# Performance work log

Hardware: AMD Instinct MI355X
Metric: run time of the kernel (lower is better)

The kernel has to match this reference:

```python
import jax, jax.numpy as jnp
import numpy as np

N_NODES = 100000
N_EDGES = 1600000
N_LABEL = 200000
IN_CH, HID_CH, OUT_CH = 64, 128, 64


def setup_inputs() -> dict:
    key = jax.random.key(0)
    ks = jax.random.split(key, 9)
    glorot = lambda k, fi, fo: jax.random.normal(k, (fi, fo), jnp.float32) * (2.0 / (fi + fo)) ** 0.5
    return {
        "x": jax.random.normal(ks[0], (N_NODES, IN_CH), jnp.float32),
        "W_l1": glorot(ks[1], IN_CH, HID_CH),
        "W_r1": glorot(ks[2], IN_CH, HID_CH),
        "b1": jnp.zeros((HID_CH,), jnp.float32),
        "W_l2": glorot(ks[3], HID_CH, OUT_CH),
        "W_r2": glorot(ks[4], HID_CH, OUT_CH),
        "b2": jnp.zeros((OUT_CH,), jnp.float32),
        "edge_index": jax.random.randint(ks[5], (2, N_EDGES), 0, N_NODES, jnp.int64 if jax.config.jax_enable_x64 else jnp.int32),
        "edge_label_index": jax.random.randint(ks[6], (2, N_LABEL), 0, N_NODES, jnp.int64 if jax.config.jax_enable_x64 else jnp.int32),
    }


def _sage_conv(x, edge_index, W_l, W_r, b):
    # PyG SAGEConv (mean aggr): out = lin_l(mean_{j in N(i)} x_j) + lin_r(x_i)
    src, dst = edge_index[0], edge_index[1]
    msg = x[src]                                             # [E, d] gather
    agg = jax.ops.segment_sum(msg, dst, num_segments=x.shape[0])  # [N, d]
    cnt = jax.ops.segment_sum(jnp.ones((edge_index.shape[1], 1), x.dtype), dst,
                              num_segments=x.shape[0])       # [N, 1]
    mean = agg / jnp.maximum(cnt, 1.0)                       # isolated nodes -> 0
    return mean @ W_l + x @ W_r + b


def reference(x, W_l1, W_r1, b1, W_l2, W_r2, b2, edge_index, edge_label_index):
    # encode (inference mode: dropout is identity)
    h = jax.nn.relu(_sage_conv(x, edge_index, W_l1, W_r1, b1))
    z = _sage_conv(h, edge_index, W_l2, W_r2, b2)            # [N, out]
    # decode: dot-product link scores
    src = z[edge_label_index[0]]                             # [P, out]
    dst = z[edge_label_index[1]]
    return jnp.sum(src * dst, axis=-1)                       # [P]
```

## Files before the change

### kernel.cpp

```cpp
#include <hip/hip_runtime.h>
#include <hip/hip_bf16.h>


#define NBUCK 512
#define NPB   200
#define WI    64

typedef __attribute__((ext_vector_type(2))) float f32x2;
typedef __attribute__((ext_vector_type(4))) float f32x4;
typedef __attribute__((ext_vector_type(4))) int i32x4;
typedef __attribute__((ext_vector_type(2))) unsigned int u32x2;
typedef __attribute__((ext_vector_type(4))) unsigned short u16x4;
typedef __attribute__((ext_vector_type(8))) unsigned short u16x8;
typedef __attribute__((ext_vector_type(8))) short s16x8;

__device__ inline unsigned short f2bf(float f) {
    unsigned u = __float_as_uint(f);
    u += 0x7fffu + ((u >> 16) & 1u);
    return (unsigned short)(u >> 16);
}
__device__ inline float bf2f(unsigned short h) {
    return __uint_as_float(((unsigned)h) << 16);
}
__device__ inline unsigned int pk4_fp8(float a, float b, float c, float d) {
    int w = __builtin_amdgcn_cvt_pk_fp8_f32(a, b, 0, false);
    w = __builtin_amdgcn_cvt_pk_fp8_f32(c, d, w, true);
    return (unsigned int)w;
}
__device__ inline unsigned char one_fp8(float a) {
    return (unsigned char)(__builtin_amdgcn_cvt_pk_fp8_f32(a, a, 0, false) & 0xFF);
}
__device__ inline void acc_fp8(unsigned int a, f32x2& lo, f32x2& hi) {
#if __has_builtin(__builtin_amdgcn_cvt_pk_f32_fp8)
    lo += __builtin_amdgcn_cvt_pk_f32_fp8((int)a, false);
    hi += __builtin_amdgcn_cvt_pk_f32_fp8((int)a, true);
#else
    lo.x += __builtin_amdgcn_cvt_f32_fp8((int)a, 0);
    lo.y += __builtin_amdgcn_cvt_f32_fp8((int)a, 1);
    hi.x += __builtin_amdgcn_cvt_f32_fp8((int)a, 2);
    hi.y += __builtin_amdgcn_cvt_f32_fp8((int)a, 3);
#endif
}

__global__ __launch_bounds__(256) void k_prep(const float* __restrict__ x,
                                              const float* __restrict__ Wl1,
                                              const float* __restrict__ Wr1,
                                              const float* __restrict__ Wl2,
                                              const float* __restrict__ Wr2,
                                              unsigned short* __restrict__ w1t,
                                              unsigned short* __restrict__ w2t,
                                              unsigned short* __restrict__ xb,
                                              unsigned int* __restrict__ xq,
                                              int* __restrict__ meta,
                                              long long nx) {
    if (blockIdx.x < 16) {
        if (blockIdx.x == 0) {
            i32x4 z = {0, 0, 0, 0};
            *(i32x4*)(meta + threadIdx.x * 4) = z;
        }
        int id = (blockIdx.x * 256 + threadIdx.x) * 8;
        int which = id >> 14;
        int r0 = id & 16383;
#pragma unroll
        for (int i = 0; i < 8; ++i) {
            int r = r0 + i;
            int n = r >> 7, k = r & 127;
            float v;
            if (which == 0) v = (k < 64) ? Wl1[k * 128 + n] : Wr1[(k - 64) * 128 + n];
            else            v = (n < 64) ? Wl2[k * 64 + n] : Wr2[k * 64 + (n - 64)];
            (which ? w2t : w1t)[r] = f2bf(v);
        }
        return;
    }
    long long i = ((long long)(blockIdx.x - 16) * 256 + threadIdx.x) * 8;
    if (i + 8 > nx) return;
    f32x4 a = __builtin_nontemporal_load((const f32x4*)(x + i));
    f32x4 b = __builtin_nontemporal_load((const f32x4*)(x + i + 4));
    u16x8 o;
    o[0] = f2bf(a.x); o[1] = f2bf(a.y); o[2] = f2bf(a.z); o[3] = f2bf(a.w);
    o[4] = f2bf(b.x); o[5] = f2bf(b.y); o[6] = f2bf(b.z); o[7] = f2bf(b.w);
    __builtin_nontemporal_store(o, (u16x8*)(xb + i));
    u32x2 q;
    q.x = pk4_fp8(a.x, a.y, a.z, a.w);
    q.y = pk4_fp8(b.x, b.y, b.z, b.w);
    __builtin_nontemporal_store(q, (u32x2*)(xq + (i >> 2)));
}

__global__ __launch_bounds__(256) void k_bucket(const int* __restrict__ ei, int E,
                                                int capB,
                                                int* __restrict__ buckets,
                                                int* __restrict__ meta,
                                                int* __restrict__ ovfA) {
    __shared__ int lcnt[NBUCK];
    __shared__ int lbase[NBUCK];
    __shared__ int lidx[NBUCK];
    const int t = threadIdx.x;
    const int e0 = blockIdx.x * 4096;
    for (int i = t; i < NBUCK; i += 256) { lcnt[i] = 0; lidx[i] = 0; }
    __syncthreads();

    int s[16], d[16], b[16];
    bool v[16];
#pragma unroll
    for (int r = 0; r < 4; ++r) {
        int e = e0 + r * 1024 + t * 4;
        i32x4 s4, d4;
        if (e + 4 <= E) {
            s4 = __builtin_nontemporal_load((const i32x4*)(ei + e));
            d4 = __builtin_nontemporal_load((const i32x4*)(ei + E + e));
        } else {
            s4.x = (e < E) ? ei[e] : 0;         d4.x = (e < E) ? ei[E + e] : 0;
            s4.y = (e + 1 < E) ? ei[e + 1] : 0; d4.y = (e + 1 < E) ? ei[E + e + 1] : 0;
            s4.z = (e + 2 < E) ? ei[e + 2] : 0; d4.z = (e + 2 < E) ? ei[E + e + 2] : 0;
            s4.w = (e + 3 < E) ? ei[e + 3] : 0; d4.w = (e + 3 < E) ? ei[E + e + 3] : 0;
        }
        s[r * 4 + 0] = s4.x; s[r * 4 + 1] = s4.y; s[r * 4 + 2] = s4.z; s[r * 4 + 3] = s4.w;
        d[r * 4 + 0] = d4.x; d[r * 4 + 1] = d4.y; d[r * 4 + 2] = d4.z; d[r * 4 + 3] = d4.w;
        v[r * 4 + 0] = (e < E); v[r * 4 + 1] = (e + 1 < E);
        v[r * 4 + 2] = (e + 2 < E); v[r * 4 + 3] = (e + 3 < E);
    }
#pragma unroll
    for (int k = 0; k < 16; ++k) {
        b[k] = (unsigned)d[k] / NPB;
        if (v[k]) atomicAdd(&lcnt[b[k]], 1);
    }
    __syncthreads();
    for (int i = t; i < NBUCK; i += 256) {
        int c = lcnt[i];
        lbase[i] = (c > 0) ? atomicAdd(&meta[i], c) : 0;
    }
    __syncthreads();
#pragma unroll
    for (int k = 0; k < 16; ++k) {
        if (!v[k]) continue;
        int slot = atomicAdd(&lidx[b[k]], 1);
        int pos = lbase[b[k]] + slot;
        if (pos < capB) {
            int local = d[k] - b[k] * NPB;
            buckets[(size_t)b[k] * capB + pos] = (local << 17) | s[k];
        } else {
            int oi = atomicAdd(&meta[NBUCK], 1);
            ovfA[(size_t)oi * 2] = s[k];
            ovfA[(size_t)oi * 2 + 1] = d[k];
        }
    }
}

__global__ __launch_bounds__(256) void k_fill_lds(const int* __restrict__ buckets,
                                                  int capB,
                                                  const int* __restrict__ meta_ro,
                                                  int* __restrict__ deg,
                                                  int* __restrict__ ell, int N) {
    __shared__ int cur[NPB];
    __shared__ int ells[NPB * WI];
    const int t = threadIdx.x;
    const int b = blockIdx.x;
    const int base = b * NPB;
    for (int i = t; i < NPB; i += 256) cur[i] = 0;
    __syncthreads();
    const int cnt = min(meta_ro[b], capB);
    const int* bk = buckets + (size_t)b * capB;
    for (int i = t; i < cnt; i += 256) {
        unsigned v = (unsigned)__builtin_nontemporal_load(bk + i);
        int s = (int)(v & 0x1FFFFu);
        int local = (int)(v >> 17);
        int slot = atomicAdd(&cur[local], 1);
        if (slot < WI) ells[local * WI + slot] = s;
    }
    __syncthreads();
    const int nn = min(NPB, N - base);
    if (nn <= 0) return;
    for (int i = t; i < nn; i += 256) deg[base + i] = cur[i];
    const int lim = nn * WI;
    for (int j = t * 4; j < lim; j += 256 * 4) {
        if ((j & (WI - 1)) >= cur[j >> 6]) continue;
        i32x4 vv = *(const i32x4*)&ells[j];
        __builtin_nontemporal_store(vv, (i32x4*)(ell + (size_t)base * WI + j));
    }
}

__global__ __launch_bounds__(256) void k_fill_list(const int* __restrict__ ovfA,
                                                   const int* __restrict__ meta_ro,
                                                   int* __restrict__ deg,
                                                   int* __restrict__ ell) {
    const int cnt = meta_ro[NBUCK];
    for (int i = blockIdx.x * 256 + threadIdx.x; i < cnt; i += gridDim.x * 256) {
        int s = ovfA[(size_t)i * 2];
        int d = ovfA[(size_t)i * 2 + 1];
        int pos = atomicAdd(&deg[d], 1);
        if (pos < WI) ell[(size_t)d * WI + pos] = s;
    }
}

__global__ __launch_bounds__(256) void k_agg_q(const unsigned int* __restrict__ featq,
                                               const int* __restrict__ deg,
                                               const int* __restrict__ ell,
                                               unsigned short* __restrict__ outb,
                                               const float* __restrict__ addend,
                                               int n) {
    const int node = blockIdx.x * 16 + (threadIdx.x >> 4);
    const int l = threadIdx.x & 15;
    if (node >= n) return;
    const int dg = deg[node];
    const int cnt = min(dg, WI);
    const int* row = ell + (size_t)node * WI;
    f32x2 lo = {0.f, 0.f}, hi = {0.f, 0.f};
    int j = 0;
    for (; j + 8 <= cnt; j += 8) {
        i32x4 sA = __builtin_nontemporal_load((const i32x4*)(row + j));
        i32x4 sB = __builtin_nontemporal_load((const i32x4*)(row + j + 4));
        unsigned a0 = featq[(size_t)sA.x * 16 + l];
        unsigned a1 = featq[(size_t)sA.y * 16 + l];
        unsigned a2 = featq[(size_t)sA.z * 16 + l];
        unsigned a3 = featq[(size_t)sA.w * 16 + l];
        unsigned a4 = featq[(size_t)sB.x * 16 + l];
        unsigned a5 = featq[(size_t)sB.y * 16 + l];
        unsigned a6 = featq[(size_t)sB.z * 16 + l];
        unsigned a7 = featq[(size_t)sB.w * 16 + l];
        acc_fp8(a0, lo, hi); acc_fp8(a1, lo, hi);
        acc_fp8(a2, lo, hi); acc_fp8(a3, lo, hi);
        acc_fp8(a4, lo, hi); acc_fp8(a5, lo, hi);
        acc_fp8(a6, lo, hi); acc_fp8(a7, lo, hi);
    }
    if (j + 4 <= cnt) {
        i32x4 sA = __builtin_nontemporal_load((const i32x4*)(row + j));
        unsigned a0 = featq[(size_t)sA.x * 16 + l];
        unsigned a1 = featq[(size_t)sA.y * 16 + l];
        unsigned a2 = featq[(size_t)sA.z * 16 + l];
        unsigned a3 = featq[(size_t)sA.w * 16 + l];
        acc_fp8(a0, lo, hi); acc_fp8(a1, lo, hi);
        acc_fp8(a2, lo, hi); acc_fp8(a3, lo, hi);
        j += 4;
    }
    for (; j < cnt; ++j) {
        int s = __builtin_nontemporal_load(row + j);
        acc_fp8(featq[(size_t)s * 16 + l], lo, hi);
    }
    const float inv = 1.0f / (float)max(dg, 1);
    float vx = lo.x * inv, vy = lo.y * inv, vz = hi.x * inv, vw = hi.y * inv;
    if (addend) {
        const f32x4 ad = *(const f32x4*)(addend + (size_t)node * 64 + l * 4);
        vx += ad.x; vy += ad.y; vz += ad.z; vw += ad.w;
    }
    u16x4 ob;
    ob[0] = f2bf(vx); ob[1] = f2bf(vy); ob[2] = f2bf(vz); ob[3] = f2bf(vw);
    __builtin_nontemporal_store(ob, (u16x4*)(outb + (size_t)node * 64 + l * 4));
}

__global__ __launch_bounds__(256) void k_gemm_fused(
    const unsigned short* __restrict__ mean1b,
    const unsigned short* __restrict__ xb,
    const unsigned short* __restrict__ w1t,
    const unsigned short* __restrict__ w2t,
    const float* __restrict__ b1,
    const float* __restrict__ b2,
    unsigned int* __restrict__ pq,
    float* __restrict__ zb, int M) {
    __shared__ unsigned short W1s[128 * 128];
    __shared__ unsigned short W2s[128 * 128];
    __shared__ __align__(16) unsigned short HT[128 * 136];
    const int t = threadIdx.x;
    const int wv = t >> 6, l = t & 63;
    const int lr = l & 15, lq = l >> 4;
    const int wrow = wv * 32;
    const int row0 = blockIdx.x * 128 + wrow;

    const s16x8 zf = {0, 0, 0, 0, 0, 0, 0, 0};
    s16x8 af[2][4];
#pragma unroll
    for (int mt = 0; mt < 2; ++mt) {
        int r = row0 + mt * 16 + lr;
        bool ok = r < M;
#pragma unroll
        for (int ks = 0; ks < 4; ++ks) {
            int k = ks * 32 + lq * 8;
            const unsigned short* src = (k < 64) ? (mean1b + (size_t)r * 64 + k)
                                                 : (xb + (size_t)r * 64 + (k - 64));
            af[mt][ks] = ok ? *(const s16x8*)src : zf;
        }
    }
#pragma unroll
    for (int i = 0; i < 8; ++i) {
        int byte = (i * 256 + t) * 16;
        int swz = byte ^ (((byte >> 8) & 7) << 4);
        *(u16x8*)((char*)W1s + swz) = *(const u16x8*)((const char*)w1t + byte);
        *(u16x8*)((char*)W2s + swz) = *(const u16x8*)((const char*)w2t + byte);
    }
    __syncthreads();
    if (row0 >= M) return;

    f32x4 acc[2][8];
#pragma unroll
    for (int mt = 0; mt < 2; ++mt)
#pragma unroll
        for (int nt = 0; nt < 8; ++nt) {
            f32x4 z = {0.f, 0.f, 0.f, 0.f};
            acc[mt][nt] = z;
        }
#pragma unroll
    for (int nt = 0; nt < 8; ++nt) {
        int n = nt * 16 + lr;
#pragma unroll
        for (int ks = 0; ks < 4; ++ks) {
            int byte = (n * 256 + ks * 64 + lq * 16) ^ ((n & 7) << 4);
            s16x8 bf = *(const s16x8*)((const char*)W1s + byte);
            acc[0][nt] = __builtin_amdgcn_mfma_f32_16x16x32_bf16(af[0][ks], bf, acc[0][nt], 0, 0, 0);
            acc[1][nt] = __builtin_amdgcn_mfma_f32_16x16x32_bf16(af[1][ks], bf, acc[1][nt], 0, 0, 0);
        }
    }
#pragma unroll
    for (int nt = 0; nt < 8; ++nt) {
        float bb = b1[nt * 16 + lr];
#pragma unroll
        for (int mt = 0; mt < 2; ++mt)
#pragma unroll
            for (int j = 0; j < 4; ++j) {
                float v = fmaxf(acc[mt][nt][j] + bb, 0.f);
                HT[(wrow + mt * 16 + lq * 4 + j) * 136 + nt * 16 + lr] = f2bf(v);
            }
    }
    s16x8 af2[2][4];
#pragma unroll
    for (int mt = 0; mt < 2; ++mt)
#pragma unroll
        for (int ks = 0; ks < 4; ++ks)
            af2[mt][ks] = *(const s16x8*)&HT[(wrow + mt * 16 + lr) * 136 + ks * 32 + lq * 8];

    f32x4 acc2[2][8];
#pragma unroll
    for (int mt = 0; mt < 2; ++mt)
#pragma unroll
        for (int nt = 0; nt < 8; ++nt) {
            f32x4 z = {0.f, 0.f, 0.f, 0.f};
            acc2[mt][nt] = z;
        }
#pragma unroll
    for (int nt = 0; nt < 8; ++nt) {
        int n = nt * 16 + lr;
#pragma unroll
        for (int ks = 0; ks < 4; ++ks) {
            int byte = (n * 256 + ks * 64 + lq * 16) ^ ((n & 7) << 4);
            s16x8 bf = *(const s16x8*)((const char*)W2s + byte);
            acc2[0][nt] = __builtin_amdgcn_mfma_f32_16x16x32_bf16(af2[0][ks], bf, acc2[0][nt], 0, 0, 0);
            acc2[1][nt] = __builtin_amdgcn_mfma_f32_16x16x32_bf16(af2[1][ks], bf, acc2[1][nt], 0, 0, 0);
        }
    }
    char* scratch = (char*)&HT[(size_t)wrow * 136];
    unsigned char* csb = (unsigned char*)scratch;
#pragma unroll
    for (int nt = 0; nt < 4; ++nt)
#pragma unroll
        for (int mt = 0; mt < 2; ++mt)
#pragma unroll
            for (int j = 0; j < 4; ++j)
                csb[(mt * 16 + lq * 4 + j) * 68 + nt * 16 + lr] = one_fp8(acc2[mt][nt][j]);
#pragma unroll
    for (int p = 0; p < 8; ++p) {
        int r = p * 4 + lq;
        int gr = row0 + r;
        if (gr < M) {
            unsigned int v = *(const unsigned int*)&csb[r * 68 + lr * 4];
            __builtin_nontemporal_store(v, pq + (size_t)gr * 16 + lr);
        }
    }
    __syncthreads();
    float* csf = (float*)scratch;
#pragma unroll
    for (int nt = 4; nt < 8; ++nt) {
        int col = (nt - 4) * 16 + lr;
        float bb = b2[col];
#pragma unroll
        for (int mt = 0; mt < 2; ++mt)
#pragma unroll
            for (int j = 0; j < 4; ++j)
                csf[(mt * 16 + lq * 4 + j) * 68 + col] = acc2[mt][nt][j] + bb;
    }
#pragma unroll
    for (int p = 0; p < 8; ++p) {
        int r = p * 4 + lq;
        int gr = row0 + r;
        if (gr < M) {
            f32x4 v = *(const f32x4*)&csf[r * 68 + lr * 4];
            __builtin_nontemporal_store(v, (f32x4*)(zb + (size_t)gr * 64 + lr * 4));
        }
    }
}

__global__ __launch_bounds__(256) void k_decode(const unsigned short* __restrict__ zq,
                                                const int* __restrict__ eli,
                                                float* __restrict__ out, int P) {
    int t = threadIdx.x;
    int g = blockIdx.x * 16 + (t >> 4);
    int l = t & 15;
    if (g >= P) return;
    int a = __builtin_nontemporal_load(eli + g);
    int b = __builtin_nontemporal_load(eli + P + g);
    u16x4 va = *(const u16x4*)(zq + (size_t)a * 64 + l * 4);
    u16x4 vb = *(const u16x4*)(zq + (size_t)b * 64 + l * 4);
    float s = bf2f(va[0]) * bf2f(vb[0]) + bf2f(va[1]) * bf2f(vb[1])
            + bf2f(va[2]) * bf2f(vb[2]) + bf2f(va[3]) * bf2f(vb[3]);
    s += __shfl_xor(s, 1);
    s += __shfl_xor(s, 2);
    s += __shfl_xor(s, 4);
    s += __shfl_xor(s, 8);
    if (l == 0) out[g] = s;
}

extern "C" void kernel_launch(void* const* d_in, const int* in_sizes, int n_in,
                              void* d_out, int out_size, void* d_ws, size_t ws_size,
                              hipStream_t stream) {
    const float* x   = (const float*)d_in[0];
    const float* Wl1 = (const float*)d_in[1];
    const float* Wr1 = (const float*)d_in[2];
    const float* b1  = (const float*)d_in[3];
    const float* Wl2 = (const float*)d_in[4];
    const float* Wr2 = (const float*)d_in[5];
    const float* b2  = (const float*)d_in[6];
    const int* ei  = (const int*)d_in[7];
    const int* eli = (const int*)d_in[8];
    const int N = in_sizes[0] / 64;
    const int E = in_sizes[7] / 2;
    const int P = in_sizes[8] / 2;
    float* out = (float*)d_out;

    const int capB = ((E / NBUCK) * 5 / 4 + 1024 + 3) & ~3;

    char* w = (char*)d_ws;
    auto alloc = [&](size_t bytes) {
        char* pp = w;
        w += (bytes + 255) & ~(size_t)255;
        return pp;
    };
    int* deg  = (int*)alloc((size_t)N * 4);
    int* meta = (int*)alloc(4096);
    int* ell  = (int*)alloc((size_t)N * WI * 4);
    unsigned short* xb     = (unsigned short*)alloc((size_t)N * 64 * 2);
    unsigned int*   xq     = (unsigned int*)alloc((size_t)N * 64);
    unsigned int*   pq     = (unsigned int*)alloc((size_t)N * 64);
    unsigned short* mean1b = (unsigned short*)alloc((size_t)N * 64 * 2);
    unsigned short* zq     = (unsigned short*)alloc((size_t)N * 64 * 2);
    unsigned short* w1t    = (unsigned short*)alloc(128 * 128 * 2);
    unsigned short* w2t    = (unsigned short*)alloc(128 * 128 * 2);
    size_t bb = (size_t)NBUCK * capB * 4 + 256 + (size_t)E * 8;
    char* breg = alloc(bb);
    int* buckets = (int*)breg;
    int* ovfA = (int*)(breg + (((size_t)NBUCK * capB * 4 + 255) & ~(size_t)255));
    float* zb = (float*)alloc((size_t)N * 64 * 4);

    {
        long long n = (long long)N * 64;
        int xblocks = (int)((n / 8 + 255) / 256);
        k_prep<<<16 + xblocks, 256, 0, stream>>>(x, Wl1, Wr1, Wl2, Wr2,
                                                 w1t, w2t, xb, xq, meta, n);
    }

    k_bucket<<<(E + 4095) / 4096, 256, 0, stream>>>(ei, E, capB, buckets, meta, ovfA);
    k_fill_lds<<<(N + NPB - 1) / NPB, 256, 0, stream>>>(buckets, capB, meta, deg, ell, N);
    k_fill_list<<<32, 256, 0, stream>>>(ovfA, meta, deg, ell);

    const int agg_grid = (N + 15) / 16;
    k_agg_q<<<agg_grid, 256, 0, stream>>>(xq, deg, ell, mean1b, nullptr, N);

    const int gemm_grid = (N + 127) / 128;
    k_gemm_fused<<<gemm_grid, 256, 0, stream>>>(mean1b, xb, w1t, w2t, b1, b2, pq, zb, N);

    k_agg_q<<<agg_grid, 256, 0, stream>>>(pq, deg, ell, zq, zb, N);

    k_decode<<<(P + 15) / 16, 256, 0, stream>>>(zq, eli, out, P);
}
```

Baseline: 155.9 us.

## Split fp8 feature tables into channel halves and aggregate each half separately

New measurement: 189.5 us. 21.6% more time.

```diff
diff --git a/kernel.cpp b/kernel.cpp
--- a/kernel.cpp
+++ b/kernel.cpp
@@ -50,7 +50,8 @@
                                               unsigned short* __restrict__ w1t,
                                               unsigned short* __restrict__ w2t,
                                               unsigned short* __restrict__ xb,
-                                              unsigned int* __restrict__ xq,
+                                              unsigned int* __restrict__ xq0,
+                                              unsigned int* __restrict__ xq1,
                                               int* __restrict__ meta,
                                               long long nx) {
     if (blockIdx.x < 16) {
@@ -83,7 +84,10 @@
     u32x2 q;
     q.x = pk4_fp8(a.x, a.y, a.z, a.w);
     q.y = pk4_fp8(b.x, b.y, b.z, b.w);
-    __builtin_nontemporal_store(q, (u32x2*)(xq + (i >> 2)));
+    long long node = i >> 6;
+    int c0 = (int)(i & 63);
+    unsigned int* xh = (c0 < 32) ? xq0 : xq1;
+    __builtin_nontemporal_store(q, (u32x2*)(xh + node * 8 + ((c0 & 31) >> 2)));
 }
 
 __global__ __launch_bounds__(256) void k_bucket(const int* __restrict__ ei, int E,
@@ -197,9 +201,9 @@
                                                const int* __restrict__ ell,
                                                unsigned short* __restrict__ outb,
                                                const float* __restrict__ addend,
-                                               int n) {
-    const int node = blockIdx.x * 16 + (threadIdx.x >> 4);
-    const int l = threadIdx.x & 15;
+                                               int n, int coff) {
+    const int node = blockIdx.x * 32 + (threadIdx.x >> 3);
+    const int l = threadIdx.x & 7;
     if (node >= n) return;
     const int dg = deg[node];
     const int cnt = min(dg, WI);
@@ -209,14 +213,14 @@
     for (; j + 8 <= cnt; j += 8) {
         i32x4 sA = __builtin_nontemporal_load((const i32x4*)(row + j));
         i32x4 sB = __builtin_nontemporal_load((const i32x4*)(row + j + 4));
-        unsigned a0 = featq[(size_t)sA.x * 16 + l];
-        unsigned a1 = featq[(size_t)sA.y * 16 + l];
-        unsigned a2 = featq[(size_t)sA.z * 16 + l];
-        unsigned a3 = featq[(size_t)sA.w * 16 + l];
-        unsigned a4 = featq[(size_t)sB.x * 16 + l];
-        unsigned a5 = featq[(size_t)sB.y * 16 + l];
-        unsigned a6 = featq[(size_t)sB.z * 16 + l];
-        unsigned a7 = featq[(size_t)sB.w * 16 + l];
+        unsigned a0 = featq[(size_t)sA.x * 8 + l];
+        unsigned a1 = featq[(size_t)sA.y * 8 + l];
+        unsigned a2 = featq[(size_t)sA.z * 8 + l];
+        unsigned a3 = featq[(size_t)sA.w * 8 + l];
+        unsigned a4 = featq[(size_t)sB.x * 8 + l];
+        unsigned a5 = featq[(size_t)sB.y * 8 + l];
+        unsigned a6 = featq[(size_t)sB.z * 8 + l];
+        unsigned a7 = featq[(size_t)sB.w * 8 + l];
         acc_fp8(a0, lo, hi); acc_fp8(a1, lo, hi);
         acc_fp8(a2, lo, hi); acc_fp8(a3, lo, hi);
         acc_fp8(a4, lo, hi); acc_fp8(a5, lo, hi);
@@ -224,27 +228,28 @@
     }
     if (j + 4 <= cnt) {
         i32x4 sA = __builtin_nontemporal_load((const i32x4*)(row + j));
-        unsigned a0 = featq[(size_t)sA.x * 16 + l];
-        unsigned a1 = featq[(size_t)sA.y * 16 + l];
-        unsigned a2 = featq[(size_t)sA.z * 16 + l];
-        unsigned a3 = featq[(size_t)sA.w * 16 + l];
+        unsigned a0 = featq[(size_t)sA.x * 8 + l];
+        unsigned a1 = featq[(size_t)sA.y * 8 + l];
+        unsigned a2 = featq[(size_t)sA.z * 8 + l];
+        unsigned a3 = featq[(size_t)sA.w * 8 + l];
         acc_fp8(a0, lo, hi); acc_fp8(a1, lo, hi);
         acc_fp8(a2, lo, hi); acc_fp8(a3, lo, hi);
         j += 4;
     }
     for (; j < cnt; ++j) {
         int s = __builtin_nontemporal_load(row + j);
-        acc_fp8(featq[(size_t)s * 16 + l], lo, hi);
+        acc_fp8(featq[(size_t)s * 8 + l], lo, hi);
     }
     const float inv = 1.0f / (float)max(dg, 1);
     float vx = lo.x * inv, vy = lo.y * inv, vz = hi.x * inv, vw = hi.y * inv;
+    const size_t o = (size_t)node * 64 + coff + l * 4;
     if (addend) {
-        const f32x4 ad = *(const f32x4*)(addend + (size_t)node * 64 + l * 4);
+        const f32x4 ad = *(const f32x4*)(addend + o);
         vx += ad.x; vy += ad.y; vz += ad.z; vw += ad.w;
     }
     u16x4 ob;
     ob[0] = f2bf(vx); ob[1] = f2bf(vy); ob[2] = f2bf(vz); ob[3] = f2bf(vw);
-    __builtin_nontemporal_store(ob, (u16x4*)(outb + (size_t)node * 64 + l * 4));
+    __builtin_nontemporal_store(ob, (u16x4*)(outb + o));
 }
 
 __global__ __launch_bounds__(256) void k_gemm_fused(
@@ -254,7 +259,8 @@
     const unsigned short* __restrict__ w2t,
     const float* __restrict__ b1,
     const float* __restrict__ b2,
-    unsigned int* __restrict__ pq,
+    unsigned int* __restrict__ pq0,
+    unsigned int* __restrict__ pq1,
     float* __restrict__ zb, int M) {
     __shared__ unsigned short W1s[128 * 128];
     __shared__ unsigned short W2s[128 * 128];
@@ -360,7 +366,9 @@
         int gr = row0 + r;
         if (gr < M) {
             unsigned int v = *(const unsigned int*)&csb[r * 68 + lr * 4];
-            __builtin_nontemporal_store(v, pq + (size_t)gr * 16 + lr);
+            unsigned int* dst = (lr < 8) ? (pq0 + (size_t)gr * 8 + lr)
+                                         : (pq1 + (size_t)gr * 8 + (lr - 8));
+            __builtin_nontemporal_store(v, dst);
         }
     }
     __syncthreads();
@@ -435,8 +443,10 @@
     int* meta = (int*)alloc(4096);
     int* ell  = (int*)alloc((size_t)N * WI * 4);
     unsigned short* xb     = (unsigned short*)alloc((size_t)N * 64 * 2);
-    unsigned int*   xq     = (unsigned int*)alloc((size_t)N * 64);
-    unsigned int*   pq     = (unsigned int*)alloc((size_t)N * 64);
+    unsigned int*   xq0    = (unsigned int*)alloc((size_t)N * 32);
+    unsigned int*   xq1    = (unsigned int*)alloc((size_t)N * 32);
+    unsigned int*   pq0    = (unsigned int*)alloc((size_t)N * 32);
+    unsigned int*   pq1    = (unsigned int*)alloc((size_t)N * 32);
     unsigned short* mean1b = (unsigned short*)alloc((size_t)N * 64 * 2);
     unsigned short* zq     = (unsigned short*)alloc((size_t)N * 64 * 2);
     unsigned short* w1t    = (unsigned short*)alloc(128 * 128 * 2);
@@ -451,20 +461,23 @@
         long long n = (long long)N * 64;
         int xblocks = (int)((n / 8 + 255) / 256);
         k_prep<<<16 + xblocks, 256, 0, stream>>>(x, Wl1, Wr1, Wl2, Wr2,
-                                                 w1t, w2t, xb, xq, meta, n);
+                                                 w1t, w2t, xb, xq0, xq1, meta, n);
     }
 
     k_bucket<<<(E + 4095) / 4096, 256, 0, stream>>>(ei, E, capB, buckets, meta, ovfA);
     k_fill_lds<<<(N + NPB - 1) / NPB, 256, 0, stream>>>(buckets, capB, meta, deg, ell, N);
     k_fill_list<<<32, 256, 0, stream>>>(ovfA, meta, deg, ell);
 
-    const int agg_grid = (N + 15) / 16;
-    k_agg_q<<<agg_grid, 256, 0, stream>>>(xq, deg, ell, mean1b, nullptr, N);
+    const int agg_grid = (N + 31) / 32;
+    k_agg_q<<<agg_grid, 256, 0, stream>>>(xq0, deg, ell, mean1b, nullptr, N, 0);
+    k_agg_q<<<agg_grid, 256, 0, stream>>>(xq1, deg, ell, mean1b, nullptr, N, 32);
 
     const int gemm_grid = (N + 127) / 128;
-    k_gemm_fused<<<gemm_grid, 256, 0, stream>>>(mean1b, xb, w1t, w2t, b1, b2, pq, zb, N);
-
-    k_agg_q<<<agg_grid, 256, 0, stream>>>(pq, deg, ell, zq, zb, N);
+    k_gemm_fused<<<gemm_grid, 256, 0, stream>>>(mean1b, xb, w1t, w2t, b1, b2,
+                                                pq0, pq1, zb, N);
+
+    k_agg_q<<<agg_grid, 256, 0, stream>>>(pq0, deg, ell, zq, zb, N, 0);
+    k_agg_q<<<agg_grid, 256, 0, stream>>>(pq1, deg, ell, zq, zb, N, 32);
 
     k_decode<<<(P + 15) / 16, 256, 0, stream>>>(zq, eli, out, P);
 }
```
